# Performance work log

Measured on AMD Instinct MI355X. Metric: run time of the kernel, lower is better.

Reference implementation:

```python
import jax, jax.numpy as jnp
import numpy as np

N_HEAD = 16
HEAD_DIM = 128  # n_embd // n_head
EPS = 1e-6
ROPE_BASE = 10000.0


def rmsnorm(x, w):
    rms = jnp.mean(x * x, axis=-1, keepdims=True)
    return w * (x * jax.lax.rsqrt(rms + EPS))


def rope_cache(T, head_dim):
    half = head_dim // 2
    inv_freq = 1.0 / (ROPE_BASE ** (jnp.arange(half, dtype=jnp.float32) / half))
    pos = jnp.arange(T, dtype=jnp.float32)
    freqs = pos[:, None] * inv_freq[None, :]  # [T, half]
    return jnp.cos(freqs), jnp.sin(freqs)


def apply_rope(x, cos, sin):
    # x: [B, H, T, D]; cos/sin: [T, D/2]
    half = x.shape[-1] // 2
    x1, x2 = x[..., :half], x[..., half:]
    return jnp.concatenate([x1 * cos - x2 * sin, x1 * sin + x2 * cos], axis=-1)


def setup_inputs() -> dict:
    key = jax.random.key(0)
    ks = jax.random.split(key, 8)
    B, T, C, Hid = 2, 2048, 2048, 5632
    s = 0.02
    return {
        "x": jax.random.normal(ks[0], (B, T, C), dtype=jnp.float32),
        "w_norm1": jnp.ones((C,), dtype=jnp.float32),
        "w_qkv": jax.random.normal(ks[1], (C, 3 * C), dtype=jnp.float32) * s,
        "w_proj": jax.random.normal(ks[2], (C, C), dtype=jnp.float32) * s,
        "w_norm2": jnp.ones((C,), dtype=jnp.float32),
        "w1": jax.random.normal(ks[3], (C, Hid), dtype=jnp.float32) * s,
        "w2": jax.random.normal(ks[4], (C, Hid), dtype=jnp.float32) * s,
        "w3": jax.random.normal(ks[5], (Hid, C), dtype=jnp.float32) * s,
    }


def reference(x, w_norm1, w_qkv, w_proj, w_norm2, w1, w2, w3):
    B, T, C = x.shape
    H, D = N_HEAD, HEAD_DIM

    # ---- attention branch ----
    h = rmsnorm(x, w_norm1)
    qkv = h @ w_qkv  # [B, T, 3C]
    q, k, v = jnp.split(qkv, 3, axis=-1)
    q = q.reshape(B, T, H, D).transpose(0, 2, 1, 3)  # [B,H,T,D]
    k = k.reshape(B, T, H, D).transpose(0, 2, 1, 3)
    v = v.reshape(B, T, H, D).transpose(0, 2, 1, 3)

    cos, sin = rope_cache(T, D)
    q = apply_rope(q, cos, sin)
    k = apply_rope(k, cos, sin)

    att = jnp.einsum('bhqd,bhkd->bhqk', q, k) / np.sqrt(D).astype(np.float32)
    causal = jnp.tril(jnp.ones((T, T), dtype=bool))
    att = jnp.where(causal, att, -jnp.inf)
    att = jax.nn.softmax(att, axis=-1)
    out = jnp.einsum('bhqk,bhkd->bhqd', att, v)
    out = out.transpose(0, 2, 1, 3).reshape(B, T, C)
    x = x + out @ w_proj

    # ---- SwiGLU MLP branch ----
    h2 = rmsnorm(x, w_norm2)
    x = x + (jax.nn.silu(h2 @ w1) * (h2 @ w2)) @ w3
    return x
```

## Files before the change

kernel.cpp:

```cpp
#include <hip/hip_runtime.h>

typedef short s16x8 __attribute__((ext_vector_type(8)));
typedef unsigned short u16;
typedef u16 u16x8 __attribute__((ext_vector_type(8)));
typedef u16 u16x4 __attribute__((ext_vector_type(4)));
typedef float f32x4 __attribute__((ext_vector_type(4)));

#define DEVINL __device__ __forceinline__

DEVINL u16 f2bf(float f) {
    unsigned u = __float_as_uint(f);
    u += 0x7FFFu + ((u >> 16) & 1u);
    return (u16)(u >> 16);
}
DEVINL float bf2f(u16 h) { return __uint_as_float((unsigned)h << 16); }

DEVINL void gl2lds16(const void* g, void* l) {
    __builtin_amdgcn_global_load_lds((const __attribute__((address_space(1))) void*)g,
                                     (__attribute__((address_space(3))) void*)l, 16, 0, 0);
}

__global__ __launch_bounds__(256) void tcast(
    const float* __restrict__ src, u16* __restrict__ dst, const int K, const int N)
{
    __shared__ float tile[32][33];
    const long k0 = (long)blockIdx.x * 32;
    const long n0 = (long)blockIdx.y * 32;
    const int tid = threadIdx.x;
    const int r = tid >> 3, c4 = (tid & 7) * 4;
    float4 v = *(const float4*)&src[(k0 + r) * N + n0 + c4];
    tile[r][c4] = v.x; tile[r][c4 + 1] = v.y; tile[r][c4 + 2] = v.z; tile[r][c4 + 3] = v.w;
    __syncthreads();
    u16x4 ov;
    ov[0] = f2bf(tile[c4][r]);     ov[1] = f2bf(tile[c4 + 1][r]);
    ov[2] = f2bf(tile[c4 + 2][r]); ov[3] = f2bf(tile[c4 + 3][r]);
    *(u16x4*)&dst[(n0 + r) * K + k0 + c4] = ov;
}

__global__ __launch_bounds__(256) void rmsnorm_cast(
    const float* __restrict__ x, const float* __restrict__ wn, u16* __restrict__ out)
{
    const int C = 2048;
    const long row = blockIdx.x;
    const int tid = threadIdx.x;
    const float4* xr = (const float4*)(x + row * C);
    float4 a = xr[tid * 2], b = xr[tid * 2 + 1];
    float ss = a.x*a.x + a.y*a.y + a.z*a.z + a.w*a.w
             + b.x*b.x + b.y*b.y + b.z*b.z + b.w*b.w;
#pragma unroll
    for (int m = 1; m < 64; m <<= 1) ss += __shfl_xor(ss, m);
    __shared__ float red[4];
    if ((tid & 63) == 0) red[tid >> 6] = ss;
    __syncthreads();
    float scale = rsqrtf((red[0] + red[1] + red[2] + red[3]) * (1.f / 2048.f) + 1e-6f);
    const float4* wr = (const float4*)wn;
    float4 wa = wr[tid * 2], wb = wr[tid * 2 + 1];
    u16x8 o;
    o[0] = f2bf(a.x * scale * wa.x); o[1] = f2bf(a.y * scale * wa.y);
    o[2] = f2bf(a.z * scale * wa.z); o[3] = f2bf(a.w * scale * wa.w);
    o[4] = f2bf(b.x * scale * wb.x); o[5] = f2bf(b.y * scale * wb.y);
    o[6] = f2bf(b.z * scale * wb.z); o[7] = f2bf(b.w * scale * wb.w);
    *(u16x8*)&out[row * C + tid * 8] = o;
}

template <int MODE>
__global__ __launch_bounds__(256, 2) void gemm128(
    const u16* __restrict__ A, const u16* __restrict__ Bt,
    const int N, const int K,
    float* __restrict__ outF, u16* __restrict__ outB,
    const float* __restrict__ resid)
{
    __shared__ u16 As[128 * 64];
    __shared__ u16 Bs[128 * 64];
    const int tid = threadIdx.x;
    const int lane = tid & 63;
    const int w = tid >> 6;
    const int wm = w >> 1, wn = w & 1;
    const int quad = lane >> 4, l16 = lane & 15;
    const long m0 = (long)blockIdx.x * 128;
    const long n0 = (long)blockIdx.y * 128;

    const u16* ga[4]; const u16* gb[4]; char* la[4]; char* lb[4];
#pragma unroll
    for (int rr = 0; rr < 4; ++rr) {
        int idx = rr * 256 + tid;
        int r = idx >> 3, j = idx & 7;
        int c = (j ^ (r & 7)) * 8;
        ga[rr] = A + (m0 + r) * K + c;
        gb[rr] = Bt + (n0 + r) * K + c;
        la[rr] = (char*)As + idx * 16;
        lb[rr] = (char*)Bs + idx * 16;
    }

    f32x4 acc[4][4] = {};

    for (int k0 = 0; k0 < K; k0 += 64) {
#pragma unroll
        for (int rr = 0; rr < 4; ++rr) {
            gl2lds16(ga[rr] + k0, la[rr]);
            gl2lds16(gb[rr] + k0, lb[rr]);
        }
        __syncthreads();
#pragma unroll
        for (int ks = 0; ks < 2; ++ks) {
            s16x8 af[4], bfv[4];
#pragma unroll
            for (int mt = 0; mt < 4; ++mt)
                af[mt] = *(const s16x8*)&As[(wm * 64 + mt * 16 + l16) * 64 +
                                            ((ks * 4 + quad) ^ (l16 & 7)) * 8];
#pragma unroll
            for (int nt = 0; nt < 4; ++nt)
                bfv[nt] = *(const s16x8*)&Bs[(wn * 64 + nt * 16 + l16) * 64 +
                                             ((ks * 4 + quad) ^ (l16 & 7)) * 8];
#pragma unroll
            for (int mt = 0; mt < 4; ++mt)
#pragma unroll
                for (int nt = 0; nt < 4; ++nt)
                    acc[mt][nt] = __builtin_amdgcn_mfma_f32_16x16x32_bf16(af[mt], bfv[nt], acc[mt][nt], 0, 0, 0);
        }
        __syncthreads();
    }

#pragma unroll
    for (int mt = 0; mt < 4; ++mt)
#pragma unroll
        for (int reg = 0; reg < 4; ++reg) {
            long row = m0 + wm * 64 + mt * 16 + quad * 4 + reg;
#pragma unroll
            for (int nt = 0; nt < 4; ++nt) {
                long col = n0 + wn * 64 + nt * 16 + l16;
                float v = acc[mt][nt][reg];
                if (MODE == 0) {
                    outB[row * N + col] = f2bf(v);
                } else {
                    outF[row * N + col] = resid[row * N + col] + v;
                }
            }
        }
}

__global__ __launch_bounds__(256, 2) void gemm_ffn(
    const u16* __restrict__ A, const u16* __restrict__ B1t, const u16* __restrict__ B2t,
    const int N, const int K, u16* __restrict__ outB)
{
    __shared__ u16 As[128 * 64];
    __shared__ u16 B1s[128 * 64];
    __shared__ u16 B2s[128 * 64];
    const int tid = threadIdx.x;
    const int lane = tid & 63;
    const int w = tid >> 6;
    const int wm = w >> 1, wn = w & 1;
    const int quad = lane >> 4, l16 = lane & 15;
    const long m0 = (long)blockIdx.x * 128;
    const long n0 = (long)blockIdx.y * 128;

    const u16* ga[4]; const u16* gb1[4]; const u16* gb2[4];
    char* la[4]; char* lb1[4]; char* lb2[4];
#pragma unroll
    for (int rr = 0; rr < 4; ++rr) {
        int idx = rr * 256 + tid;
        int r = idx >> 3, j = idx & 7;
        int c = (j ^ (r & 7)) * 8;
        ga[rr]  = A + (m0 + r) * K + c;
        gb1[rr] = B1t + (n0 + r) * K + c;
        gb2[rr] = B2t + (n0 + r) * K + c;
        la[rr]  = (char*)As + idx * 16;
        lb1[rr] = (char*)B1s + idx * 16;
        lb2[rr] = (char*)B2s + idx * 16;
    }

    f32x4 acc1[4][4] = {};
    f32x4 acc2[4][4] = {};

    for (int k0 = 0; k0 < K; k0 += 64) {
#pragma unroll
        for (int rr = 0; rr < 4; ++rr) {
            gl2lds16(ga[rr] + k0, la[rr]);
            gl2lds16(gb1[rr] + k0, lb1[rr]);
            gl2lds16(gb2[rr] + k0, lb2[rr]);
        }
        __syncthreads();
#pragma unroll
        for (int ks = 0; ks < 2; ++ks) {
            s16x8 af[4], b1f[4], b2f[4];
#pragma unroll
            for (int mt = 0; mt < 4; ++mt)
                af[mt] = *(const s16x8*)&As[(wm * 64 + mt * 16 + l16) * 64 +
                                            ((ks * 4 + quad) ^ (l16 & 7)) * 8];
#pragma unroll
            for (int nt = 0; nt < 4; ++nt) {
                b1f[nt] = *(const s16x8*)&B1s[(wn * 64 + nt * 16 + l16) * 64 +
                                              ((ks * 4 + quad) ^ (l16 & 7)) * 8];
                b2f[nt] = *(const s16x8*)&B2s[(wn * 64 + nt * 16 + l16) * 64 +
                                              ((ks * 4 + quad) ^ (l16 & 7)) * 8];
            }
#pragma unroll
            for (int mt = 0; mt < 4; ++mt)
#pragma unroll
                for (int nt = 0; nt < 4; ++nt) {
                    acc1[mt][nt] = __builtin_amdgcn_mfma_f32_16x16x32_bf16(af[mt], b1f[nt], acc1[mt][nt], 0, 0, 0);
                    acc2[mt][nt] = __builtin_amdgcn_mfma_f32_16x16x32_bf16(af[mt], b2f[nt], acc2[mt][nt], 0, 0, 0);
                }
        }
        __syncthreads();
    }

#pragma unroll
    for (int mt = 0; mt < 4; ++mt)
#pragma unroll
        for (int reg = 0; reg < 4; ++reg) {
            long row = m0 + wm * 64 + mt * 16 + quad * 4 + reg;
#pragma unroll
            for (int nt = 0; nt < 4; ++nt) {
                long col = n0 + wn * 64 + nt * 16 + l16;
                float g = acc1[mt][nt][reg];
                float s = g / (1.f + __expf(-g));
                outB[row * N + col] = f2bf(s * acc2[mt][nt][reg]);
            }
        }
}

__global__ __launch_bounds__(256) void rope_qk(
    const u16* __restrict__ qkv, u16* __restrict__ qT, u16* __restrict__ kT)
{
    const int row = blockIdx.x;
    const int t = row & 2047, b = row >> 11;
    const int tid = threadIdx.x;
    __shared__ u16 buf[4096];
    const u16* src = qkv + (long)row * 6144;
    u16x8 aa = *(const u16x8*)&src[tid * 8];
    u16x8 kk = *(const u16x8*)&src[2048 + tid * 8];
    *(u16x8*)&buf[tid * 8] = aa;
    *(u16x8*)&buf[2048 + tid * 8] = kk;
    __syncthreads();
    const int c = tid * 8;
    const int h = c >> 7, dh = c & 127;
    const bool first = dh < 64;
    const int pc = first ? (c + 64) : (c - 64);
    float cs[8], sn[8];
#pragma unroll
    for (int j = 0; j < 8; ++j) {
        float inv = __expf(-(float)((dh & 63) + j) * 0.14391156831212787f);
        float ang = (float)t * inv;
        cs[j] = cosf(ang); sn[j] = sinf(ang);
    }
    const long obase = ((long)(b * 16 + h) * 2048 + t) * 128 + dh;
#pragma unroll
    for (int part = 0; part < 2; ++part) {
        const int base = part * 2048;
        u16x8 mine = *(const u16x8*)&buf[base + c];
        u16x8 oth  = *(const u16x8*)&buf[base + pc];
        const float qs = part ? 1.f : 0.08838834764831845f;
        u16x8 o;
#pragma unroll
        for (int j = 0; j < 8; ++j) {
            float xv = bf2f(mine[j]), yv = bf2f(oth[j]);
            float ov = first ? (xv * cs[j] - yv * sn[j]) : (yv * sn[j] + xv * cs[j]);
            o[j] = f2bf(ov * qs);
        }
        u16* dst = part ? kT : qT;
        *(u16x8*)&dst[obase] = o;
    }
}

__global__ __launch_bounds__(256) void vtrans(
    const u16* __restrict__ qkv, u16* __restrict__ vT)
{
    const int bh = blockIdx.x;
    const int b = bh >> 4, h = bh & 15;
    const int t0 = blockIdx.y * 64, d0 = blockIdx.z * 64;
    __shared__ u16 tile[64 * 65];
    const int tid = threadIdx.x;
#pragma unroll
    for (int rr = 0; rr < 2; ++rr) {
        int idx = rr * 256 + tid;
        int r = idx >> 3, c = (idx & 7) * 8;
        u16x8 v = *(const u16x8*)&qkv[(long)(b * 2048 + t0 + r) * 6144 + 4096 + h * 128 + d0 + c];
#pragma unroll
        for (int j = 0; j < 8; ++j) tile[r * 65 + c + j] = v[j];
    }
    __syncthreads();
#pragma unroll
    for (int rr = 0; rr < 2; ++rr) {
        int idx = rr * 256 + tid;
        int dd = idx >> 3, cc = (idx & 7) * 8;
        u16x8 o;
#pragma unroll
        for (int j = 0; j < 8; ++j) o[j] = tile[(cc + j) * 65 + dd];
        *(u16x8*)&vT[((long)bh * 128 + d0 + dd) * 2048 + t0 + cc] = o;
    }
}

__global__ __launch_bounds__(256, 2) void attn_kernel(
    const u16* __restrict__ qT, const u16* __restrict__ kT,
    const u16* __restrict__ vT, u16* __restrict__ outT)
{
    const int T = 2048, D = 128;
    const int qt = gridDim.x - 1 - blockIdx.x;
    const int bh = blockIdx.y;
    const int tid = threadIdx.x, lane = tid & 63, w = tid >> 6;
    const int quad = lane >> 4, l16 = lane & 15;
    const int qrow = qt * 64 + w * 16;

    __shared__ u16 Ks[2][64 * 128];
    __shared__ u16 Vs[2][128 * 64];
    __shared__ u16 Ps[4][16 * 64];

    s16x8 aq[4];
    const u16* qb = qT + ((long)bh * T + qrow + l16) * D;
#pragma unroll
    for (int kk = 0; kk < 4; ++kk)
        aq[kk] = *(const s16x8*)&qb[kk * 32 + quad * 8];

    f32x4 o[8] = {};
    float mi[4] = {-INFINITY, -INFINITY, -INFINITY, -INFINITY};
    float li[4] = {0.f, 0.f, 0.f, 0.f};

    const u16* kg0 = kT + (long)bh * T * D;
    const u16* vg0 = vT + (long)bh * D * T;

    auto stage = [&](int kt, int b) {
        const int k0 = kt * 64;
#pragma unroll
        for (int rr = 0; rr < 4; ++rr) {
            int idx = rr * 256 + tid;
            int kr = idx >> 4, kj = idx & 15;
            gl2lds16(kg0 + (long)(k0 + kr) * D + ((kj ^ (kr & 15)) * 8),
                     (char*)Ks[b] + idx * 16);
            int vr = idx >> 3, vj = idx & 7;
            gl2lds16(vg0 + (long)vr * T + k0 + ((vj ^ (vr & 7)) * 8),
                     (char*)Vs[b] + idx * 16);
        }
    };

    stage(0, 0);

    for (int kt = 0; kt <= qt; ++kt) {
        __syncthreads();
        if (kt < qt) stage(kt + 1, (kt + 1) & 1);
        const u16* ks_ = Ks[kt & 1];
        const u16* vs_ = Vs[kt & 1];
        const int k0 = kt * 64;

        f32x4 sf[4] = {};
#pragma unroll
        for (int kk = 0; kk < 4; ++kk) {
#pragma unroll
            for (int nt = 0; nt < 4; ++nt) {
                s16x8 kb = *(const s16x8*)&ks_[(nt * 16 + l16) * 128 +
                                               ((kk * 4 + quad) ^ (l16 & 15)) * 8];
                sf[nt] = __builtin_amdgcn_mfma_f32_16x16x32_bf16(aq[kk], kb, sf[nt], 0, 0, 0);
            }
        }

        float S[4][4];
        if (kt == qt) {
#pragma unroll
            for (int nt = 0; nt < 4; ++nt) {
                int col = k0 + nt * 16 + l16;
#pragma unroll
                for (int reg = 0; reg < 4; ++reg) {
                    int row = qrow + quad * 4 + reg;
                    S[nt][reg] = (col <= row) ? sf[nt][reg] : -INFINITY;
                }
            }
        } else {
#pragma unroll
            for (int nt = 0; nt < 4; ++nt)
#pragma unroll
                for (int reg = 0; reg < 4; ++reg)
                    S[nt][reg] = sf[nt][reg];
        }

        float rm[4];
#pragma unroll
        for (int reg = 0; reg < 4; ++reg)
            rm[reg] = fmaxf(fmaxf(S[0][reg], S[1][reg]), fmaxf(S[2][reg], S[3][reg]));
#pragma unroll
        for (int m = 1; m < 16; m <<= 1)
#pragma unroll
            for (int reg = 0; reg < 4; ++reg)
                rm[reg] = fmaxf(rm[reg], __shfl_xor(rm[reg], m));

        float alpha[4], rs[4];
#pragma unroll
        for (int reg = 0; reg < 4; ++reg) {
            float mn = fmaxf(mi[reg], rm[reg]);
            alpha[reg] = __expf(mi[reg] - mn);
            mi[reg] = mn;
            rs[reg] = 0.f;
        }
#pragma unroll
        for (int nt = 0; nt < 4; ++nt)
#pragma unroll
            for (int reg = 0; reg < 4; ++reg) {
                float p = __expf(S[nt][reg] - mi[reg]);
                S[nt][reg] = p;
                rs[reg] += p;
            }
#pragma unroll
        for (int m = 1; m < 16; m <<= 1)
#pragma unroll
            for (int reg = 0; reg < 4; ++reg)
                rs[reg] += __shfl_xor(rs[reg], m);
#pragma unroll
        for (int reg = 0; reg < 4; ++reg)
            li[reg] = li[reg] * alpha[reg] + rs[reg];
#pragma unroll
        for (int dt = 0; dt < 8; ++dt)
#pragma unroll
            for (int reg = 0; reg < 4; ++reg)
                o[dt][reg] *= alpha[reg];

#pragma unroll
        for (int nt = 0; nt < 4; ++nt)
#pragma unroll
            for (int reg = 0; reg < 4; ++reg) {
                int prow = quad * 4 + reg;
                int pcol = nt * 16 + l16;
                Ps[w][prow * 64 + (((pcol >> 3) ^ (prow & 7)) * 8) + (pcol & 7)]
                    = f2bf(S[nt][reg]);
            }

#pragma unroll
        for (int ks = 0; ks < 2; ++ks) {
            s16x8 pa = *(const s16x8*)&Ps[w][l16 * 64 +
                                             ((ks * 4 + quad) ^ (l16 & 7)) * 8];
#pragma unroll
            for (int dt = 0; dt < 8; ++dt) {
                s16x8 vb = *(const s16x8*)&vs_[(dt * 16 + l16) * 64 +
                                               ((ks * 4 + quad) ^ (l16 & 7)) * 8];
                o[dt] = __builtin_amdgcn_mfma_f32_16x16x32_bf16(pa, vb, o[dt], 0, 0, 0);
            }
        }
    }

    const int b = bh >> 4, h = bh & 15;
#pragma unroll
    for (int reg = 0; reg < 4; ++reg) {
        float inv = 1.f / li[reg];
        int t = qrow + quad * 4 + reg;
        u16* orow = outT + ((long)(b * T + t)) * 2048 + h * 128;
#pragma unroll
        for (int dt = 0; dt < 8; ++dt)
            orow[dt * 16 + l16] = f2bf(o[dt][reg] * inv);
    }
}

extern "C" void kernel_launch(void* const* d_in, const int* in_sizes, int n_in,
                              void* d_out, int out_size, void* d_ws, size_t ws_size,
                              hipStream_t stream) {
    const float* x      = (const float*)d_in[0];
    const float* wn1    = (const float*)d_in[1];
    const float* w_qkv  = (const float*)d_in[2];
    const float* w_proj = (const float*)d_in[3];
    const float* wn2    = (const float*)d_in[4];
    const float* w1     = (const float*)d_in[5];
    const float* w2     = (const float*)d_in[6];
    const float* w3     = (const float*)d_in[7];
    float* out = (float*)d_out;

    char* p = (char*)d_ws;
    u16* Z       = (u16*)p; p += (size_t)6144 * 2048 * 2;
    u16* wproj_t = (u16*)p; p += (size_t)2048 * 2048 * 2;
    u16* w1_t    = (u16*)p; p += (size_t)5632 * 2048 * 2;
    u16* w2_t    = (u16*)p; p += (size_t)5632 * 2048 * 2;
    u16* C       = (u16*)p; p += (size_t)4096 * 2048 * 2;
    u16* D       = (u16*)p; p += (size_t)4096 * 6144 * 2;
    u16* E       = (u16*)p; p += (size_t)3 * 32 * 2048 * 128 * 2;

    u16* wqkv_t = Z;
    u16* w3_t   = Z;
    u16* qT = E;
    u16* kT = E + (size_t)32 * 2048 * 128;
    u16* vT = E + (size_t)2 * 32 * 2048 * 128;
    float* x2 = (float*)E;
    u16* uu = D;

    tcast<<<dim3(64, 192), 256, 0, stream>>>(w_qkv, wqkv_t, 2048, 6144);
    tcast<<<dim3(64, 64), 256, 0, stream>>>(w_proj, wproj_t, 2048, 2048);
    tcast<<<dim3(64, 176), 256, 0, stream>>>(w1, w1_t, 2048, 5632);
    tcast<<<dim3(64, 176), 256, 0, stream>>>(w2, w2_t, 2048, 5632);

    rmsnorm_cast<<<4096, 256, 0, stream>>>(x, wn1, C);
    gemm128<0><<<dim3(32, 48), 256, 0, stream>>>(C, wqkv_t, 6144, 2048,
                                                 nullptr, D, nullptr);
    rope_qk<<<4096, 256, 0, stream>>>(D, qT, kT);
    vtrans<<<dim3(32, 32, 2), 256, 0, stream>>>(D, vT);

    tcast<<<dim3(176, 64), 256, 0, stream>>>(w3, w3_t, 5632, 2048);

    attn_kernel<<<dim3(32, 32), 256, 0, stream>>>(qT, kT, vT, C);

    gemm128<1><<<dim3(32, 16), 256, 0, stream>>>(C, wproj_t, 2048, 2048,
                                                 x2, nullptr, x);
    rmsnorm_cast<<<4096, 256, 0, stream>>>(x2, wn2, C);
    gemm_ffn<<<dim3(32, 44), 256, 0, stream>>>(C, w1_t, w2_t, 5632, 2048, uu);
    gemm128<1><<<dim3(32, 16), 256, 0, stream>>>(uu, w3_t, 2048, 5632,
                                                 out, nullptr, x2);
}
```

Measured before the change: 871.1 us.

## Double attention query tile per block and add lazy softmax rescaling

Each attention block now handles 128 query rows, with each wave owning two 16-row MFMA tiles, so every K/V tile staged in LDS serves twice as many queries and the grid halves. It also skips the running-max update and rescaling of the output accumulators when the new row max exceeds the stored max by no more than 8, a standard lazy-rescale trick that keeps results exact because the final normalisation uses the same stale max. The cost is more accumulator registers per thread, fewer blocks to spread the causal imbalance across, and extra masking work on the two diagonal tiles.

New measurement: 889.0 us. 2.1% more time.

```diff
diff --git a/kernel.cpp b/kernel.cpp
--- a/kernel.cpp
+++ b/kernel.cpp
@@ -300,21 +300,27 @@
     const int bh = blockIdx.y;
     const int tid = threadIdx.x, lane = tid & 63, w = tid >> 6;
     const int quad = lane >> 4, l16 = lane & 15;
-    const int qrow = qt * 64 + w * 16;
+    const int qrow = qt * 128 + w * 32;
 
     __shared__ u16 Ks[2][64 * 128];
     __shared__ u16 Vs[2][128 * 64];
-    __shared__ u16 Ps[4][16 * 64];
-
-    s16x8 aq[4];
-    const u16* qb = qT + ((long)bh * T + qrow + l16) * D;
-#pragma unroll
-    for (int kk = 0; kk < 4; ++kk)
-        aq[kk] = *(const s16x8*)&qb[kk * 32 + quad * 8];
-
-    f32x4 o[8] = {};
-    float mi[4] = {-INFINITY, -INFINITY, -INFINITY, -INFINITY};
-    float li[4] = {0.f, 0.f, 0.f, 0.f};
+    __shared__ u16 Ps[4][32 * 64];
+
+    s16x8 aq[2][4];
+#pragma unroll
+    for (int rt = 0; rt < 2; ++rt) {
+        const u16* qb = qT + ((long)bh * T + qrow + rt * 16 + l16) * D;
+#pragma unroll
+        for (int kk = 0; kk < 4; ++kk)
+            aq[rt][kk] = *(const s16x8*)&qb[kk * 32 + quad * 8];
+    }
+
+    f32x4 o[2][8] = {};
+    float mi[2][4], li[2][4];
+#pragma unroll
+    for (int rt = 0; rt < 2; ++rt)
+#pragma unroll
+        for (int r = 0; r < 4; ++r) { mi[rt][r] = -INFINITY; li[rt][r] = 0.f; }
 
     const u16* kg0 = kT + (long)bh * T * D;
     const u16* vg0 = vT + (long)bh * D * T;
@@ -333,118 +339,157 @@
         }
     };
 
+    const int nkt = 2 * qt + 2;
     stage(0, 0);
 
-    for (int kt = 0; kt <= qt; ++kt) {
+    for (int kt = 0; kt < nkt; ++kt) {
         __syncthreads();
-        if (kt < qt) stage(kt + 1, (kt + 1) & 1);
+        if (kt + 1 < nkt) stage(kt + 1, (kt + 1) & 1);
         const u16* ks_ = Ks[kt & 1];
         const u16* vs_ = Vs[kt & 1];
         const int k0 = kt * 64;
 
-        f32x4 sf[4] = {};
+        f32x4 sf[2][4] = {};
 #pragma unroll
         for (int kk = 0; kk < 4; ++kk) {
 #pragma unroll
             for (int nt = 0; nt < 4; ++nt) {
                 s16x8 kb = *(const s16x8*)&ks_[(nt * 16 + l16) * 128 +
                                                ((kk * 4 + quad) ^ (l16 & 15)) * 8];
-                sf[nt] = __builtin_amdgcn_mfma_f32_16x16x32_bf16(aq[kk], kb, sf[nt], 0, 0, 0);
+                sf[0][nt] = __builtin_amdgcn_mfma_f32_16x16x32_bf16(aq[0][kk], kb, sf[0][nt], 0, 0, 0);
+                sf[1][nt] = __builtin_amdgcn_mfma_f32_16x16x32_bf16(aq[1][kk], kb, sf[1][nt], 0, 0, 0);
             }
         }
 
-        float S[4][4];
-        if (kt == qt) {
-#pragma unroll
-            for (int nt = 0; nt < 4; ++nt) {
-                int col = k0 + nt * 16 + l16;
+        float S[2][4][4];
+        if (kt >= 2 * qt) {
+#pragma unroll
+            for (int rt = 0; rt < 2; ++rt)
+#pragma unroll
+                for (int nt = 0; nt < 4; ++nt) {
+                    int col = k0 + nt * 16 + l16;
+#pragma unroll
+                    for (int reg = 0; reg < 4; ++reg) {
+                        int row = qrow + rt * 16 + quad * 4 + reg;
+                        S[rt][nt][reg] = (col <= row) ? sf[rt][nt][reg] : -INFINITY;
+                    }
+                }
+        } else {
+#pragma unroll
+            for (int rt = 0; rt < 2; ++rt)
+#pragma unroll
+                for (int nt = 0; nt < 4; ++nt)
+#pragma unroll
+                    for (int reg = 0; reg < 4; ++reg)
+                        S[rt][nt][reg] = sf[rt][nt][reg];
+        }
+
+        float rm[2][4];
+#pragma unroll
+        for (int rt = 0; rt < 2; ++rt)
+#pragma unroll
+            for (int reg = 0; reg < 4; ++reg)
+                rm[rt][reg] = fmaxf(fmaxf(S[rt][0][reg], S[rt][1][reg]),
+                                    fmaxf(S[rt][2][reg], S[rt][3][reg]));
+#pragma unroll
+        for (int m = 1; m < 16; m <<= 1)
+#pragma unroll
+            for (int rt = 0; rt < 2; ++rt)
+#pragma unroll
+                for (int reg = 0; reg < 4; ++reg)
+                    rm[rt][reg] = fmaxf(rm[rt][reg], __shfl_xor(rm[rt][reg], m));
+
+        int cond = 1;
+#pragma unroll
+        for (int rt = 0; rt < 2; ++rt)
+#pragma unroll
+            for (int reg = 0; reg < 4; ++reg)
+                cond &= (rm[rt][reg] - mi[rt][reg] <= 8.f) ? 1 : 0;
+        if (!__all(cond)) {
+            float alpha[2][4];
+#pragma unroll
+            for (int rt = 0; rt < 2; ++rt)
 #pragma unroll
                 for (int reg = 0; reg < 4; ++reg) {
-                    int row = qrow + quad * 4 + reg;
-                    S[nt][reg] = (col <= row) ? sf[nt][reg] : -INFINITY;
+                    float mn = fmaxf(mi[rt][reg], rm[rt][reg]);
+                    float al = __expf(mi[rt][reg] - mn);
+                    mi[rt][reg] = mn;
+                    li[rt][reg] *= al;
+                    alpha[rt][reg] = al;
                 }
-            }
-        } else {
+#pragma unroll
+            for (int rt = 0; rt < 2; ++rt)
+#pragma unroll
+                for (int dt = 0; dt < 8; ++dt)
+#pragma unroll
+                    for (int reg = 0; reg < 4; ++reg)
+                        o[rt][dt][reg] *= alpha[rt][reg];
+        }
+
+        float rs[2][4] = {};
+#pragma unroll
+        for (int rt = 0; rt < 2; ++rt)
 #pragma unroll
             for (int nt = 0; nt < 4; ++nt)
 #pragma unroll
+                for (int reg = 0; reg < 4; ++reg) {
+                    float p = __expf(S[rt][nt][reg] - mi[rt][reg]);
+                    S[rt][nt][reg] = p;
+                    rs[rt][reg] += p;
+                }
+#pragma unroll
+        for (int m = 1; m < 16; m <<= 1)
+#pragma unroll
+            for (int rt = 0; rt < 2; ++rt)
+#pragma unroll
                 for (int reg = 0; reg < 4; ++reg)
-                    S[nt][reg] = sf[nt][reg];
-        }
-
-        float rm[4];
-#pragma unroll
-        for (int reg = 0; reg < 4; ++reg)
-            rm[reg] = fmaxf(fmaxf(S[0][reg], S[1][reg]), fmaxf(S[2][reg], S[3][reg]));
-#pragma unroll
-        for (int m = 1; m < 16; m <<= 1)
+                    rs[rt][reg] += __shfl_xor(rs[rt][reg], m);
+#pragma unroll
+        for (int rt = 0; rt < 2; ++rt)
 #pragma unroll
             for (int reg = 0; reg < 4; ++reg)
-                rm[reg] = fmaxf(rm[reg], __shfl_xor(rm[reg], m));
-
-        float alpha[4], rs[4];
-#pragma unroll
-        for (int reg = 0; reg < 4; ++reg) {
-            float mn = fmaxf(mi[reg], rm[reg]);
-            alpha[reg] = __expf(mi[reg] - mn);
-            mi[reg] = mn;
-            rs[reg] = 0.f;
-        }
-#pragma unroll
-        for (int nt = 0; nt < 4; ++nt)
-#pragma unroll
-            for (int reg = 0; reg < 4; ++reg) {
-                float p = __expf(S[nt][reg] - mi[reg]);
-                S[nt][reg] = p;
-                rs[reg] += p;
-            }
-#pragma unroll
-        for (int m = 1; m < 16; m <<= 1)
-#pragma unroll
-            for (int reg = 0; reg < 4; ++reg)
-                rs[reg] += __shfl_xor(rs[reg], m);
-#pragma unroll
-        for (int reg = 0; reg < 4; ++reg)
-            li[reg] = li[reg] * alpha[reg] + rs[reg];
-#pragma unroll
-        for (int dt = 0; dt < 8; ++dt)
-#pragma unroll
-            for (int reg = 0; reg < 4; ++reg)
-                o[dt][reg] *= alpha[reg];
-
-#pragma unroll
-        for (int nt = 0; nt < 4; ++nt)
-#pragma unroll
-            for (int reg = 0; reg < 4; ++reg) {
-                int prow = quad * 4 + reg;
-                int pcol = nt * 16 + l16;
-                Ps[w][prow * 64 + (((pcol >> 3) ^ (prow & 7)) * 8) + (pcol & 7)]
-                    = f2bf(S[nt][reg]);
-            }
+                li[rt][reg] += rs[rt][reg];
+
+#pragma unroll
+        for (int rt = 0; rt < 2; ++rt)
+#pragma unroll
+            for (int nt = 0; nt < 4; ++nt)
+#pragma unroll
+                for (int reg = 0; reg < 4; ++reg) {
+                    int prow = rt * 16 + quad * 4 + reg;
+                    int pcol = nt * 16 + l16;
+                    Ps[w][prow * 64 + (((pcol >> 3) ^ (prow & 7)) * 8) + (pcol & 7)]
+                        = f2bf(S[rt][nt][reg]);
+                }
 
 #pragma unroll
         for (int ks = 0; ks < 2; ++ks) {
-            s16x8 pa = *(const s16x8*)&Ps[w][l16 * 64 +
-                                             ((ks * 4 + quad) ^ (l16 & 7)) * 8];
+            s16x8 pa0 = *(const s16x8*)&Ps[w][l16 * 64 +
+                                              ((ks * 4 + quad) ^ (l16 & 7)) * 8];
+            s16x8 pa1 = *(const s16x8*)&Ps[w][(16 + l16) * 64 +
+                                              ((ks * 4 + quad) ^ (l16 & 7)) * 8];
 #pragma unroll
             for (int dt = 0; dt < 8; ++dt) {
                 s16x8 vb = *(const s16x8*)&vs_[(dt * 16 + l16) * 64 +
                                                ((ks * 4 + quad) ^ (l16 & 7)) * 8];
-                o[dt] = __builtin_amdgcn_mfma_f32_16x16x32_bf16(pa, vb, o[dt], 0, 0, 0);
+                o[0][dt] = __builtin_amdgcn_mfma_f32_16x16x32_bf16(pa0, vb, o[0][dt], 0, 0, 0);
+                o[1][dt] = __builtin_amdgcn_mfma_f32_16x16x32_bf16(pa1, vb, o[1][dt], 0, 0, 0);
             }
         }
     }
 
     const int b = bh >> 4, h = bh & 15;
 #pragma unroll
-    for (int reg = 0; reg < 4; ++reg) {
-        float inv = 1.f / li[reg];
-        int t = qrow + quad * 4 + reg;
-        u16* orow = outT + ((long)(b * T + t)) * 2048 + h * 128;
-#pragma unroll
-        for (int dt = 0; dt < 8; ++dt)
-            orow[dt * 16 + l16] = f2bf(o[dt][reg] * inv);
-    }
+    for (int rt = 0; rt < 2; ++rt)
+#pragma unroll
+        for (int reg = 0; reg < 4; ++reg) {
+            float inv = 1.f / li[rt][reg];
+            int t = qrow + rt * 16 + quad * 4 + reg;
+            u16* orow = outT + ((long)(b * T + t)) * 2048 + h * 128;
+#pragma unroll
+            for (int dt = 0; dt < 8; ++dt)
+                orow[dt * 16 + l16] = f2bf(o[rt][dt][reg] * inv);
+        }
 }
 
 extern "C" void kernel_launch(void* const* d_in, const int* in_sizes, int n_in,
@@ -490,7 +535,7 @@
 
     tcast<<<dim3(176, 64), 256, 0, stream>>>(w3, w3_t, 5632, 2048);
 
-    attn_kernel<<<dim3(32, 32), 256, 0, stream>>>(qT, kT, vT, C);
+    attn_kernel<<<dim3(16, 32), 256, 0, stream>>>(qT, kT, vT, C);
 
     gemm128<1><<<dim3(32, 16), 256, 0, stream>>>(C, wproj_t, 2048, 2048,
                                                  x2, nullptr, x);
```
